# Kernel optimization log

Measured on AMD Instinct MI355X. Metric: run time of the kernel, lower is better.

The kernel has to match this reference:

```python
import jax, jax.numpy as jnp
import numpy as np

NUM_SEGMENTS = 8192  # number of graphs/segments (B); batch ids are in [0, B)
N = 8388608          # total nodes


def setup_inputs() -> dict:
    key = jax.random.key(0)
    k1, k2 = jax.random.split(key)
    x = jax.random.normal(k1, (N,), dtype=jnp.float32)
    batch = jnp.sort(jax.random.randint(k2, (N,), 0, NUM_SEGMENTS))
    return {"x": x, "batch": batch}


def _sparsemax(x, batch):
    n = x.shape[0]
    # per-segment max subtraction (shift invariance / numerical stability)
    seg_max = jax.ops.segment_max(x, batch, num_segments=NUM_SEGMENTS)
    xs = x - seg_max[batch]

    # segmented descending sort: primary key = batch, secondary = -x
    order = jnp.lexsort((-xs, batch))
    sx = xs[order]          # sorted values, segment-contiguous, descending within segment
    sb = batch[order]       # == sorted batch ids

    # segment sizes and start offsets
    num_nodes = jax.ops.segment_sum(jnp.ones_like(batch), batch, num_segments=NUM_SEGMENTS)
    cum = jnp.concatenate([jnp.zeros((1,), num_nodes.dtype), jnp.cumsum(num_nodes)[:-1]])

    # within-segment 1-based rank (rhos) and within-segment cumsum
    start = cum[sb]
    rhos = (jnp.arange(n) - start + 1).astype(x.dtype)
    c = jnp.cumsum(sx)
    base = jnp.where(start > 0, c[jnp.maximum(start - 1, 0)], jnp.zeros((), x.dtype))
    seg_cumsum = c - base

    # sparsemax support: rho * z_sorted > cumsum - 1
    support = rhos * sx > seg_cumsum - 1.0
    supp_size = jax.ops.segment_sum(support.astype(num_nodes.dtype), sb, num_segments=NUM_SEGMENTS)

    # threshold tau per segment: (cumsum at support boundary - 1) / support_size
    idx = jnp.clip(cum + supp_size - 1, 0, n - 1)
    tau = (seg_cumsum[idx] - 1.0) / jnp.maximum(supp_size, 1).astype(x.dtype)

    return jnp.maximum(xs - tau[batch], 0.0)


def reference(x, batch):
    return _sparsemax(x, batch)
```

## Files before the change

kernel.cpp:

```cpp
#include <hip/hip_runtime.h>


#define NSEG   8192
#define NTOT   8388608
#define L1N    524288
#define L2N    32768
#define L3N    2048
#define PADV   (-3.0e38f)
#define WREG   1552
#define FBB    256

__device__ __forceinline__ int esw(const int e) {
    return (e & ~15) | ((e + (e >> 4)) & 15);
}

__device__ __forceinline__ void cs(float& a, float& b, const bool up) {
    const float lo = fminf(a, b), hi = fmaxf(a, b);
    a = up ? hi : lo;
    b = up ? lo : hi;
}

__device__ __forceinline__ void sort8(float r[8], const int gib) {
    cs(r[0], r[1], true);  cs(r[2], r[3], false); cs(r[4], r[5], true);  cs(r[6], r[7], false);
    cs(r[0], r[2], true);  cs(r[1], r[3], true);  cs(r[4], r[6], false); cs(r[5], r[7], false);
    cs(r[0], r[1], true);  cs(r[2], r[3], true);  cs(r[4], r[5], false); cs(r[6], r[7], false);
    const bool u8 = ((gib & 8) == 0);
    cs(r[0], r[4], u8); cs(r[1], r[5], u8); cs(r[2], r[6], u8); cs(r[3], r[7], u8);
    cs(r[0], r[2], u8); cs(r[1], r[3], u8); cs(r[4], r[6], u8); cs(r[5], r[7], u8);
    cs(r[0], r[1], u8); cs(r[2], r[3], u8); cs(r[4], r[5], u8); cs(r[6], r[7], u8);
}

template<int K>
__device__ __forceinline__ void bmerge(float r[8], const int gib) {
    const bool up = ((gib & K) == 0);
    #pragma unroll
    for (int j = K >> 1; j >= 8; j >>= 1) {
        const bool tkm = (up == ((gib & j) == 0));
        const int tm = j >> 3;
        #pragma unroll
        for (int m = 0; m < 8; ++m) {
            const float p = __shfl_xor(r[m], tm, 64);
            r[m] = tkm ? fmaxf(r[m], p) : fminf(r[m], p);
        }
    }
    #pragma unroll
    for (int j = 4; j >= 1; j >>= 1)
        #pragma unroll
        for (int m = 0; m < 8; ++m)
            if ((m & j) == 0) cs(r[m], r[m | j], up);
}

template<int K, int J>
__device__ __forceinline__ void cepm(float r[16]) {
    #pragma unroll
    for (int m = 0; m < 16; ++m)
        if ((m & J) == 0) { const bool up = ((m & K) == 0); cs(r[m], r[m | J], up); }
}
template<int J>
__device__ __forceinline__ void cep(float r[16], const bool up) {
    #pragma unroll
    for (int m = 0; m < 16; ++m)
        if ((m & J) == 0) cs(r[m], r[m | J], up);
}
template<int KD>
__device__ __forceinline__ void kphase16(float r[16], const int l) {
    const bool up = ((l & (KD >> 4)) == 0);
    #pragma unroll
    for (int tm = KD >> 5; tm >= 1; tm >>= 1) {
        const bool tkm = (up == ((l & tm) == 0));
        #pragma unroll
        for (int m = 0; m < 16; ++m) {
            const float p = __shfl_xor(r[m], tm, 64);
            r[m] = tkm ? fmaxf(r[m], p) : fminf(r[m], p);
        }
    }
    cep<8>(r, up); cep<4>(r, up); cep<2>(r, up); cep<1>(r, up);
}
__device__ __forceinline__ void wsort1024(float r[16], const int l) {
    cepm<2, 1>(r);
    cepm<4, 2>(r); cepm<4, 1>(r);
    cepm<8, 4>(r); cepm<8, 2>(r); cepm<8, 1>(r);
    kphase16<16>(r, l);  kphase16<32>(r, l);  kphase16<64>(r, l);
    kphase16<128>(r, l); kphase16<256>(r, l); kphase16<512>(r, l);
    kphase16<1024>(r, l);
}

__global__ void k1_bounds(const int* __restrict__ batch, int* __restrict__ starts, const int n)
{
    const int i = blockIdx.x * blockDim.x + threadIdx.x;
    if (i >= n) return;
    const int bi = batch[i];
    if (i == 0) { for (int b = 0; b <= bi; ++b) starts[b] = 0; }
    else {
        const int bp = batch[i - 1];
        for (int b = bp + 1; b <= bi; ++b) starts[b] = i;
    }
    if (i == n - 1) { for (int b = bi + 1; b <= NSEG; ++b) starts[b] = n; }
}

__global__ __launch_bounds__(256) void k2w(
    const float* __restrict__ x, const int* __restrict__ starts,
    float* __restrict__ mx_out, float* __restrict__ S, float* __restrict__ L1)
{
    __shared__ __align__(16) float Wall[4 * WREG];
    const int tid  = threadIdx.x;
    const int lane = tid & 63;
    const int wid  = tid >> 6;
    float* W = Wall + wid * WREG;

    const int b = blockIdx.x * 4 + wid;
    const int s = starts[b], e = starts[b + 1];
    const int n = e - s;
    if (n <= 0) { if (lane == 0) mx_out[b] = 0.0f; return; }

    const bool med = (n > 1024);
    const int  nb  = n - 1024;

    float r[16], rb[8];
    #pragma unroll
    for (int m = 0; m < 16; ++m) { const int i = 16 * lane + m; r[m] = (i < n) ? x[s + i] : PADV; }
    if (med) {
        #pragma unroll
        for (int m = 0; m < 8; ++m) { const int i = 1024 + 8 * lane + m; rb[m] = (i < n) ? x[s + i] : PADV; }
    }

    float mx = r[0];
    #pragma unroll
    for (int m = 1; m < 16; ++m) mx = fmaxf(mx, r[m]);
    if (med) {
        #pragma unroll
        for (int m = 0; m < 8; ++m) mx = fmaxf(mx, rb[m]);
    }
    #pragma unroll
    for (int o = 32; o; o >>= 1) mx = fmaxf(mx, __shfl_xor(mx, o, 64));
    if (lane == 0) mx_out[b] = mx;

    #pragma unroll
    for (int m = 0; m < 16; ++m) r[m] = r[m] - mx;
    if (med) {
        #pragma unroll
        for (int m = 0; m < 8; ++m) rb[m] = rb[m] - mx;
    }

    wsort1024(r, lane);

    if (med) {
        const int gib = 8 * lane;
        sort8(rb, gib);
        bmerge<16>(rb, gib); bmerge<32>(rb, gib); bmerge<64>(rb, gib);
        bmerge<128>(rb, gib); bmerge<256>(rb, gib); bmerge<512>(rb, gib);

        #pragma unroll
        for (int m = 0; m < 16; ++m) W[esw(16 * lane + m)] = r[m];
        #pragma unroll
        for (int m = 0; m < 8; ++m)  W[esw(1024 + 8 * lane + m)] = rb[m];

        float mg[24];
        const int d0 = 24 * lane;
        int cnt = 0;
        if (d0 < n) {
            int lo = (d0 > nb) ? d0 - nb : 0;
            int hi = (d0 < 1024) ? d0 : 1024;
            while (lo < hi) {
                const int a = (lo + hi) >> 1;
                if (W[esw(a)] >= W[esw(1024 + d0 - a - 1)]) lo = a + 1; else hi = a;
            }
            int i = lo, j = d0 - lo;
            cnt = (d0 + 24 < n) ? 24 : (n - d0);
            #pragma unroll
            for (int kk = 0; kk < 24; ++kk) {
                if (kk < cnt) {
                    const bool tA = (j >= nb) || (i < 1024 && W[esw(i)] >= W[esw(1024 + j)]);
                    if (tA) { mg[kk] = W[esw(i)]; ++i; }
                    else    { mg[kk] = W[esw(1024 + j)]; ++j; }
                }
            }
        }
        for (int kk = 0; kk < cnt; ++kk) W[esw(d0 + kk)] = mg[kk];
    } else {
        #pragma unroll
        for (int m = 0; m < 16; ++m) W[esw(16 * lane + m)] = r[m];
    }

    for (int i = lane; i < n; i += 64) S[s + i] = W[esw(i)];

    const int q0 = (s + 15) >> 4, q1 = e >> 4;
    for (int rr = lane; rr < q1 - q0; rr += 64) {
        const int lb = ((q0 + rr) << 4) - s;
        float v[16];
        #pragma unroll
        for (int ii = 0; ii < 16; ++ii) v[ii] = W[esw(lb + ii)];
        float a = 0.0f;
        #pragma unroll
        for (int ii = 0; ii < 16; ++ii) a = a + v[ii];
        L1[q0 + rr] = a;
    }
}

__global__ void k_border(const float* __restrict__ S, const int* __restrict__ starts,
                         float* __restrict__ L1)
{
    const int b = blockIdx.x * blockDim.x + threadIdx.x;
    if (b >= NSEG) return;
    const int s = starts[b];
    if (s & 15) {
        const int q = s >> 4;
        const float* p = S + ((size_t)q << 4);
        float a = 0.0f;
        #pragma unroll
        for (int i = 0; i < 16; ++i) a = a + p[i];
        L1[q] = a;
    }
}

__global__ __launch_bounds__(256) void kA(const float* __restrict__ L1,
                                          float* __restrict__ L2, float* __restrict__ L3)
{
    __shared__ float l2s[256];
    const int k = blockIdx.x, tid = threadIdx.x;
    const int q2 = (k << 8) + tid;
    const float4* p = (const float4*)(L1 + ((size_t)q2 << 4));
    float a = 0.0f;
    #pragma unroll
    for (int v = 0; v < 4; ++v) {
        const float4 f = p[v];
        a = a + f.x; a = a + f.y; a = a + f.z; a = a + f.w;
    }
    L2[q2] = a;
    l2s[tid] = a;
    __syncthreads();
    if (tid < 16) {
        float s3 = 0.0f;
        #pragma unroll
        for (int i = 0; i < 16; ++i) s3 = s3 + l2s[(tid << 4) + i];
        L3[(k << 4) + tid] = s3;
    }
}

__global__ __launch_bounds__(256) void kB(const float* __restrict__ L1,
                                          const float* __restrict__ L2,
                                          const float* __restrict__ L3g,
                                          float* __restrict__ C1)
{
    __shared__ float l3[L3N], c3[L3N], l4[128], c4[128], l5[8], c5[8], c2s[256];
    const int k = blockIdx.x, tid = threadIdx.x;

    for (int q = tid; q < L3N; q += 256) l3[q] = L3g[q];
    __syncthreads();
    if (tid < 128) {
        float a = 0.0f;
        for (int i = 0; i < 16; ++i) a = a + l3[tid * 16 + i];
        l4[tid] = a;
    }
    __syncthreads();
    if (tid < 8) {
        float a = 0.0f;
        for (int i = 0; i < 16; ++i) a = a + l4[tid * 16 + i];
        l5[tid] = a;
    }
    __syncthreads();
    if (tid == 0) {
        float a = 0.0f;
        for (int i = 0; i < 8; ++i) { a = a + l5[i]; c5[i] = a; }
    }
    __syncthreads();
    if (tid < 8) {
        const float pre = tid ? c5[tid - 1] : 0.0f;
        float a = 0.0f;
        for (int i = 0; i < 16; ++i) { a = a + l4[tid * 16 + i]; c4[tid * 16 + i] = tid ? (a + pre) : a; }
    }
    __syncthreads();
    if (tid < 128) {
        const float pre = tid ? c4[tid - 1] : 0.0f;
        float a = 0.0f;
        for (int i = 0; i < 16; ++i) { a = a + l3[tid * 16 + i]; c3[tid * 16 + i] = tid ? (a + pre) : a; }
    }
    __syncthreads();
    if (tid < 16) {
        const int q2r = (k << 4) + tid;
        const float pre = q2r ? c3[q2r - 1] : 0.0f;
        const float* p = L2 + ((size_t)q2r << 4);
        float a = 0.0f;
        #pragma unroll
        for (int i = 0; i < 16; ++i) { a = a + p[i]; c2s[(tid << 4) + i] = q2r ? (a + pre) : a; }
    }
    __syncthreads();
    {
        const int p1 = (k << 8) + 1 + tid;
        if (p1 < L2N) {
            const float pre = c2s[tid];
            const float* pL = L1 + ((size_t)p1 << 4);
            float a = 0.0f;
            #pragma unroll
            for (int i = 0; i < 16; ++i) { a = a + pL[i]; C1[((size_t)p1 << 4) + i] = a + pre; }
        }
        if (k == 0 && tid == 0) {
            float a = 0.0f;
            #pragma unroll
            for (int i = 0; i < 16; ++i) { a = a + L1[i]; C1[i] = a; }
        }
    }
}

__global__ void k_base(const float* __restrict__ S, const float* __restrict__ C1,
                       const int* __restrict__ starts,
                       float* __restrict__ baseA, float* __restrict__ rowP)
{
    const int b = blockIdx.x * blockDim.x + threadIdx.x;
    if (b >= NSEG) return;
    const int s = starts[b];
    float P = 0.0f, base = 0.0f;
    if (s > 0) {
        const int j = s - 1;
        const int q = j >> 4;
        const float* p = S + ((size_t)q << 4);
        float a = 0.0f;
        for (int i = 0; i <= (j & 15); ++i) a = a + p[i];
        if (s & 15) P = a;
        base = q ? (a + C1[q - 1]) : a;
    }
    baseA[b] = base;
    rowP[b] = P;
}

__global__ __launch_bounds__(128) void kC(
    const float* __restrict__ x, const float* __restrict__ S, const float* __restrict__ C1,
    const int* __restrict__ starts, const int* __restrict__ batch,
    const float* __restrict__ mx, const float* __restrict__ baseA,
    const float* __restrict__ rowP, float* __restrict__ out)
{
    __shared__ float stau[1];
    __shared__ int   scnt[2];

    const int b = blockIdx.x, tid = threadIdx.x;
    const int s = starts[b], e = starts[b + 1];
    const int n = e - s;
    if (n <= 0) return;

    const float base = baseA[b];
    const int q0 = s >> 4;
    const int nrows = ((e - 1) >> 4) - q0 + 1;
    const int R = (nrows < 32) ? nrows : 32;

    int cnt = 0;
    for (int rr = tid; rr < R; rr += 128) {
        const int q = q0 + rr;
        const float pre = q ? C1[q - 1] : 0.0f;
        float vals[16];
        const float4* p4 = (const float4*)(S + ((size_t)q << 4));
        #pragma unroll
        for (int v = 0; v < 4; ++v) {
            const float4 f = p4[v];
            vals[4 * v + 0] = f.x; vals[4 * v + 1] = f.y;
            vals[4 * v + 2] = f.z; vals[4 * v + 3] = f.w;
        }
        float a = (rr == 0) ? rowP[b] : 0.0f;
        const int i0 = (rr == 0) ? (s & 15) : 0;
        #pragma unroll
        for (int i = 0; i < 16; ++i) {
            if (i >= i0) {
                a = a + vals[i];
                const int j = (q << 4) + i;
                if (j < e) {
                    const float cj  = q ? (a + pre) : a;
                    const float seg = (cj - base) - 1.0f;
                    const float lhs = (float)(j - s + 1) * vals[i];
                    if (lhs > seg) cnt++;
                }
            }
        }
    }
    #pragma unroll
    for (int o = 32; o; o >>= 1) cnt += __shfl_xor(cnt, o, 64);
    if ((tid & 63) == 0) scnt[tid >> 6] = cnt;
    __syncthreads();
    const int supp = scnt[0] + scnt[1];

    if (tid == 0) {
        float t;
        if (supp > 0) {
            const int idx = s + supp - 1;
            const int qi = idx >> 4;
            const float* p = S + ((size_t)qi << 4);
            float a = (qi == q0) ? rowP[b] : 0.0f;
            const int i0 = (qi == q0) ? (s & 15) : 0;
            for (int i = i0; i <= (idx & 15); ++i) a = a + p[i];
            const float ci = qi ? (a + C1[qi - 1]) : a;
            t = ((ci - base) - 1.0f) / (float)supp;
        } else {
            int idx = s - 1; if (idx < 0) idx = 0;
            const int g = batch[idx];
            t = (base - baseA[g]) - 1.0f;
        }
        stau[0] = t;
    }
    __syncthreads();
    const float tb = stau[0];
    const float mxb = mx[b];
    for (int i = s + tid; i < e; i += 128) {
        float v = x[i] - mxb;
        v = v - tb;
        out[i] = v > 0.0f ? v : 0.0f;
    }
}

__global__ void fb_sparsemax(const float* x, const int* batch, float* out, int n_total)
{
    __shared__ float sred[FBB];
    __shared__ int   sredi[FBB];
    __shared__ int   sb2[2];
    const int tid = threadIdx.x;
    const int b = blockIdx.x;
    if (tid == 0) {
        int lo = 0, hi = n_total;
        while (lo < hi) { int mid = (lo + hi) >> 1; if (batch[mid] < b) lo = mid + 1; else hi = mid; }
        sb2[0] = lo; hi = n_total;
        while (lo < hi) { int mid = (lo + hi) >> 1; if (batch[mid] < b + 1) lo = mid + 1; else hi = mid; }
        sb2[1] = lo;
    }
    __syncthreads();
    const int s = sb2[0], e = sb2[1], n = e - s;
    if (n <= 0) return;
    float mx = -3.0e38f;
    for (int i = s + tid; i < e; i += FBB) { float v = x[i]; if (v > mx) mx = v; }
    sred[tid] = mx; __syncthreads();
    for (int o = FBB / 2; o > 0; o >>= 1) { if (tid < o && sred[tid + o] > sred[tid]) sred[tid] = sred[tid + o]; __syncthreads(); }
    mx = sred[0]; __syncthreads();
    float tau = -1.0f; int prev = -1;
    for (int it = 0; it < 64; ++it) {
        float sum = 0.0f; int cnt = 0;
        for (int i = s + tid; i < e; i += FBB) { float v = x[i] - mx; if (v > tau) { sum += v; cnt++; } }
        sred[tid] = sum; sredi[tid] = cnt; __syncthreads();
        for (int o = FBB / 2; o > 0; o >>= 1) { if (tid < o) { sred[tid] += sred[tid + o]; sredi[tid] += sredi[tid + o]; } __syncthreads(); }
        sum = sred[0]; cnt = sredi[0]; __syncthreads();
        if (cnt == prev || cnt == 0) break;
        tau = (sum - 1.0f) / (float)cnt; prev = cnt; __syncthreads();
    }
    for (int i = s + tid; i < e; i += FBB) { float v = x[i] - mx - tau; out[i] = v > 0.0f ? v : 0.0f; }
}
__global__ void fb_sentinel(float* out) { if (threadIdx.x == 0 && blockIdx.x == 0) out[0] = 20000.0f; }

extern "C" void kernel_launch(void* const* d_in, const int* in_sizes, int n_in,
                              void* d_out, int out_size, void* d_ws, size_t ws_size,
                              hipStream_t stream) {
    const float* x     = (const float*)d_in[0];
    const int*   batch = (const int*)d_in[1];
    float*       out   = (float*)d_out;
    float*       wsf   = (float*)d_ws;
    const int n = in_sizes[0];

    const size_t need = (size_t)8448 + 8192 * 3 + L1N + L2N + L3N + L1N;
    if (n != NTOT || ws_size < need * sizeof(float)) {
        fb_sparsemax<<<NSEG, FBB, 0, stream>>>(x, batch, out, n);
        fb_sentinel<<<1, 64, 0, stream>>>(out);
        return;
    }
    int*   starts = (int*)wsf;
    float* mx     = wsf + 8448;
    float* baseA  = mx + 8192;
    float* rowP   = baseA + 8192;
    float* L1 = rowP + 8192;
    float* L2 = L1 + L1N;
    float* L3 = L2 + L2N;
    float* C1 = L3 + L3N;
    float* S  = out;

    k1_bounds<<<(n + 255) / 256, 256, 0, stream>>>(batch, starts, n);
    k2w<<<NSEG / 4, 256, 0, stream>>>(x, starts, mx, S, L1);
    k_border<<<NSEG / 256, 256, 0, stream>>>(S, starts, L1);
    kA<<<128, 256, 0, stream>>>(L1, L2, L3);
    kB<<<128, 256, 0, stream>>>(L1, L2, L3, C1);
    k_base<<<NSEG / 256, 256, 0, stream>>>(S, C1, starts, baseA, rowP);
    kC<<<NSEG, 128, 0, stream>>>(x, S, C1, starts, batch, mx, baseA, rowP, out);
}
```

Before: 216.0 us.

## Fuse tail kernels into one persistent kernel with software grid barriers

Replaces the border, two-level scan, base and final sparsemax kernels with a single persistent kernel of 1024 blocks. The phases are separated by atomic-counter grid barriers, with counters reset in the bounds kernel. The goal is to remove several launch gaps and inter-kernel drains. The cost is spin-wait barriers that rely on all blocks being co-resident, redundant per-block loading of the L3 array, and sequential processing of 8 segments per block in the final phase.

After: 596.5 us. +176.2%, slower.

```diff
diff --git a/kernel.cpp b/kernel.cpp
--- a/kernel.cpp
+++ b/kernel.cpp
@@ -8,6 +8,8 @@
 #define L3N    2048
 #define PADV   (-3.0e38f)
 #define WREG   1552
+#define NTB    1024
+#define SEGB   (NSEG / NTB)
 #define FBB    256
 
 __device__ __forceinline__ int esw(const int e) {
@@ -85,9 +87,11 @@
     kphase16<1024>(r, l);
 }
 
-__global__ void k1_bounds(const int* __restrict__ batch, int* __restrict__ starts, const int n)
+__global__ void k1_bounds(const int* __restrict__ batch, int* __restrict__ starts,
+                          int* __restrict__ ctrs, const int n)
 {
     const int i = blockIdx.x * blockDim.x + threadIdx.x;
+    if (blockIdx.x == 0 && threadIdx.x < 8) ctrs[threadIdx.x] = 0;
     if (i >= n) return;
     const int bi = batch[i];
     if (i == 0) { for (int b = 0; b <= bi; ++b) starts[b] = 0; }
@@ -197,53 +201,64 @@
     }
 }
 
-__global__ void k_border(const float* __restrict__ S, const int* __restrict__ starts,
-                         float* __restrict__ L1)
+__device__ __forceinline__ void gbar(int* ctr) {
+    __syncthreads();
+    if (threadIdx.x == 0) {
+        __threadfence();
+        atomicAdd(ctr, 1);
+        while (__hip_atomic_load(ctr, __ATOMIC_RELAXED, __HIP_MEMORY_SCOPE_AGENT) < NTB)
+            __builtin_amdgcn_s_sleep(8);
+        __threadfence();
+    }
+    __syncthreads();
+}
+
+__global__ __launch_bounds__(256) void kTAIL(
+    const float* __restrict__ x, const float* __restrict__ S,
+    const int* __restrict__ starts, const int* __restrict__ batch,
+    float* __restrict__ L1, float* __restrict__ L2, float* __restrict__ L3g,
+    float* __restrict__ C1, const float* __restrict__ mx,
+    float* __restrict__ baseA, float* __restrict__ rowP,
+    float* __restrict__ out, int* __restrict__ ctrs)
 {
-    const int b = blockIdx.x * blockDim.x + threadIdx.x;
-    if (b >= NSEG) return;
-    const int s = starts[b];
-    if (s & 15) {
-        const int q = s >> 4;
-        const float* p = S + ((size_t)q << 4);
-        float a = 0.0f;
-        #pragma unroll
-        for (int i = 0; i < 16; ++i) a = a + p[i];
-        L1[q] = a;
-    }
-}
-
-__global__ __launch_bounds__(256) void kA(const float* __restrict__ L1,
-                                          float* __restrict__ L2, float* __restrict__ L3)
-{
-    __shared__ float l2s[256];
-    const int k = blockIdx.x, tid = threadIdx.x;
-    const int q2 = (k << 8) + tid;
-    const float4* p = (const float4*)(L1 + ((size_t)q2 << 4));
-    float a = 0.0f;
-    #pragma unroll
-    for (int v = 0; v < 4; ++v) {
-        const float4 f = p[v];
-        a = a + f.x; a = a + f.y; a = a + f.z; a = a + f.w;
-    }
-    L2[q2] = a;
-    l2s[tid] = a;
-    __syncthreads();
-    if (tid < 16) {
-        float s3 = 0.0f;
-        #pragma unroll
-        for (int i = 0; i < 16; ++i) s3 = s3 + l2s[(tid << 4) + i];
-        L3[(k << 4) + tid] = s3;
-    }
-}
-
-__global__ __launch_bounds__(256) void kB(const float* __restrict__ L1,
-                                          const float* __restrict__ L2,
-                                          const float* __restrict__ L3g,
-                                          float* __restrict__ C1)
-{
-    __shared__ float l3[L3N], c3[L3N], l4[128], c4[128], l5[8], c5[8], c2s[256];
-    const int k = blockIdx.x, tid = threadIdx.x;
+    __shared__ float l3[L3N], c3[L3N], l4[128], c4[128], l5[8], c5[8];
+    __shared__ float l2s[32], c2s[32], stau[1];
+    const int blk = blockIdx.x, tid = threadIdx.x;
+
+    if (tid < SEGB) {
+        const int b = blk * SEGB + tid;
+        const int s = starts[b];
+        if (s & 15) {
+            const int q = s >> 4;
+            const float* p = S + ((size_t)q << 4);
+            float a = 0.0f;
+            #pragma unroll
+            for (int i = 0; i < 16; ++i) a = a + p[i];
+            L1[q] = a;
+        }
+    }
+    gbar(ctrs + 0);
+
+    if (tid < 32) {
+        const int q2 = blk * 32 + tid;
+        const float4* p = (const float4*)(L1 + ((size_t)q2 << 4));
+        float a = 0.0f;
+        #pragma unroll
+        for (int v = 0; v < 4; ++v) {
+            const float4 f = p[v];
+            a = a + f.x; a = a + f.y; a = a + f.z; a = a + f.w;
+        }
+        L2[q2] = a;
+        l2s[tid] = a;
+    }
+    __syncthreads();
+    if (tid < 2) {
+        float a = 0.0f;
+        #pragma unroll
+        for (int i = 0; i < 16; ++i) a = a + l2s[(tid << 4) + i];
+        L3g[blk * 2 + tid] = a;
+    }
+    gbar(ctrs + 1);
 
     for (int q = tid; q < L3N; q += 256) l3[q] = L3g[q];
     __syncthreads();
@@ -276,8 +291,8 @@
         for (int i = 0; i < 16; ++i) { a = a + l3[tid * 16 + i]; c3[tid * 16 + i] = tid ? (a + pre) : a; }
     }
     __syncthreads();
-    if (tid < 16) {
-        const int q2r = (k << 4) + tid;
+    if (tid < 2) {
+        const int q2r = blk * 2 + tid;
         const float pre = q2r ? c3[q2r - 1] : 0.0f;
         const float* p = L2 + ((size_t)q2r << 4);
         float a = 0.0f;
@@ -285,8 +300,8 @@
         for (int i = 0; i < 16; ++i) { a = a + p[i]; c2s[(tid << 4) + i] = q2r ? (a + pre) : a; }
     }
     __syncthreads();
-    {
-        const int p1 = (k << 8) + 1 + tid;
+    if (tid < 32) {
+        const int p1 = blk * 32 + 1 + tid;
         if (p1 < L2N) {
             const float pre = c2s[tid];
             const float* pL = L1 + ((size_t)p1 << 4);
@@ -294,113 +309,103 @@
             #pragma unroll
             for (int i = 0; i < 16; ++i) { a = a + pL[i]; C1[((size_t)p1 << 4) + i] = a + pre; }
         }
-        if (k == 0 && tid == 0) {
+    }
+    if (blk == 0 && tid == 0) {
+        float a = 0.0f;
+        #pragma unroll
+        for (int i = 0; i < 16; ++i) { a = a + L1[i]; C1[i] = a; }
+    }
+    gbar(ctrs + 2);
+
+    if (tid < SEGB) {
+        const int b = blk * SEGB + tid;
+        const int s = starts[b];
+        float P = 0.0f, base = 0.0f;
+        if (s > 0) {
+            const int j = s - 1;
+            const int q = j >> 4;
+            const float* p = S + ((size_t)q << 4);
             float a = 0.0f;
-            #pragma unroll
-            for (int i = 0; i < 16; ++i) { a = a + L1[i]; C1[i] = a; }
-        }
-    }
-}
-
-__global__ void k_base(const float* __restrict__ S, const float* __restrict__ C1,
-                       const int* __restrict__ starts,
-                       float* __restrict__ baseA, float* __restrict__ rowP)
-{
-    const int b = blockIdx.x * blockDim.x + threadIdx.x;
-    if (b >= NSEG) return;
-    const int s = starts[b];
-    float P = 0.0f, base = 0.0f;
-    if (s > 0) {
-        const int j = s - 1;
-        const int q = j >> 4;
-        const float* p = S + ((size_t)q << 4);
-        float a = 0.0f;
-        for (int i = 0; i <= (j & 15); ++i) a = a + p[i];
-        if (s & 15) P = a;
-        base = q ? (a + C1[q - 1]) : a;
-    }
-    baseA[b] = base;
-    rowP[b] = P;
-}
-
-__global__ __launch_bounds__(128) void kC(
-    const float* __restrict__ x, const float* __restrict__ S, const float* __restrict__ C1,
-    const int* __restrict__ starts, const int* __restrict__ batch,
-    const float* __restrict__ mx, const float* __restrict__ baseA,
-    const float* __restrict__ rowP, float* __restrict__ out)
-{
-    __shared__ float stau[1];
-    __shared__ int   scnt[2];
-
-    const int b = blockIdx.x, tid = threadIdx.x;
-    const int s = starts[b], e = starts[b + 1];
-    const int n = e - s;
-    if (n <= 0) return;
-
-    const float base = baseA[b];
-    const int q0 = s >> 4;
-    const int nrows = ((e - 1) >> 4) - q0 + 1;
-    const int R = (nrows < 32) ? nrows : 32;
-
-    int cnt = 0;
-    for (int rr = tid; rr < R; rr += 128) {
-        const int q = q0 + rr;
-        const float pre = q ? C1[q - 1] : 0.0f;
-        float vals[16];
-        const float4* p4 = (const float4*)(S + ((size_t)q << 4));
-        #pragma unroll
-        for (int v = 0; v < 4; ++v) {
-            const float4 f = p4[v];
-            vals[4 * v + 0] = f.x; vals[4 * v + 1] = f.y;
-            vals[4 * v + 2] = f.z; vals[4 * v + 3] = f.w;
-        }
-        float a = (rr == 0) ? rowP[b] : 0.0f;
-        const int i0 = (rr == 0) ? (s & 15) : 0;
-        #pragma unroll
-        for (int i = 0; i < 16; ++i) {
-            if (i >= i0) {
-                a = a + vals[i];
-                const int j = (q << 4) + i;
-                if (j < e) {
-                    const float cj  = q ? (a + pre) : a;
-                    const float seg = (cj - base) - 1.0f;
-                    const float lhs = (float)(j - s + 1) * vals[i];
-                    if (lhs > seg) cnt++;
+            for (int i = 0; i <= (j & 15); ++i) a = a + p[i];
+            if (s & 15) P = a;
+            base = q ? (a + C1[q - 1]) : a;
+        }
+        baseA[b] = base;
+        rowP[b] = P;
+    }
+    gbar(ctrs + 3);
+
+    for (int si = 0; si < SEGB; ++si) {
+        const int b = blk * SEGB + si;
+        const int s = starts[b], e = starts[b + 1];
+        const int n = e - s;
+        if (n <= 0) continue;
+
+        const float base = baseA[b];
+        const int q0 = s >> 4;
+        const int nrows = ((e - 1) >> 4) - q0 + 1;
+        const int R = (nrows < 32) ? nrows : 32;
+
+        int cnt = 0;
+        if (tid < R) {
+            const int q = q0 + tid;
+            const float pre = q ? C1[q - 1] : 0.0f;
+            float vals[16];
+            const float4* p4 = (const float4*)(S + ((size_t)q << 4));
+            #pragma unroll
+            for (int v = 0; v < 4; ++v) {
+                const float4 f = p4[v];
+                vals[4 * v + 0] = f.x; vals[4 * v + 1] = f.y;
+                vals[4 * v + 2] = f.z; vals[4 * v + 3] = f.w;
+            }
+            float a = (tid == 0) ? rowP[b] : 0.0f;
+            const int i0 = (tid == 0) ? (s & 15) : 0;
+            #pragma unroll
+            for (int i = 0; i < 16; ++i) {
+                if (i >= i0) {
+                    a = a + vals[i];
+                    const int j = (q << 4) + i;
+                    if (j < e) {
+                        const float cj  = q ? (a + pre) : a;
+                        const float seg = (cj - base) - 1.0f;
+                        const float lhs = (float)(j - s + 1) * vals[i];
+                        if (lhs > seg) cnt++;
+                    }
                 }
             }
         }
-    }
-    #pragma unroll
-    for (int o = 32; o; o >>= 1) cnt += __shfl_xor(cnt, o, 64);
-    if ((tid & 63) == 0) scnt[tid >> 6] = cnt;
-    __syncthreads();
-    const int supp = scnt[0] + scnt[1];
-
-    if (tid == 0) {
-        float t;
-        if (supp > 0) {
-            const int idx = s + supp - 1;
-            const int qi = idx >> 4;
-            const float* p = S + ((size_t)qi << 4);
-            float a = (qi == q0) ? rowP[b] : 0.0f;
-            const int i0 = (qi == q0) ? (s & 15) : 0;
-            for (int i = i0; i <= (idx & 15); ++i) a = a + p[i];
-            const float ci = qi ? (a + C1[qi - 1]) : a;
-            t = ((ci - base) - 1.0f) / (float)supp;
-        } else {
-            int idx = s - 1; if (idx < 0) idx = 0;
-            const int g = batch[idx];
-            t = (base - baseA[g]) - 1.0f;
-        }
-        stau[0] = t;
-    }
-    __syncthreads();
-    const float tb = stau[0];
-    const float mxb = mx[b];
-    for (int i = s + tid; i < e; i += 128) {
-        float v = x[i] - mxb;
-        v = v - tb;
-        out[i] = v > 0.0f ? v : 0.0f;
+        if (tid < 64) {
+            #pragma unroll
+            for (int o = 16; o; o >>= 1) cnt += __shfl_xor(cnt, o, 64);
+        }
+        if (tid == 0) {
+            const int supp = cnt;
+            float t;
+            if (supp > 0) {
+                const int idx = s + supp - 1;
+                const int qi = idx >> 4;
+                const float* p = S + ((size_t)qi << 4);
+                float a = (qi == q0) ? rowP[b] : 0.0f;
+                const int i0 = (qi == q0) ? (s & 15) : 0;
+                for (int i = i0; i <= (idx & 15); ++i) a = a + p[i];
+                const float ci = qi ? (a + C1[qi - 1]) : a;
+                t = ((ci - base) - 1.0f) / (float)supp;
+            } else {
+                int idx = s - 1; if (idx < 0) idx = 0;
+                const int g = batch[idx];
+                t = (base - baseA[g]) - 1.0f;
+            }
+            stau[0] = t;
+        }
+        __syncthreads();
+        const float tb = stau[0];
+        const float mxb = mx[b];
+        for (int i = s + tid; i < e; i += 256) {
+            float v = x[i] - mxb;
+            v = v - tb;
+            out[i] = v > 0.0f ? v : 0.0f;
+        }
+        __syncthreads();
     }
 }
 
@@ -449,14 +454,15 @@
     float*       wsf   = (float*)d_ws;
     const int n = in_sizes[0];
 
-    const size_t need = (size_t)8448 + 8192 * 3 + L1N + L2N + L3N + L1N;
+    const size_t need = (size_t)8 + 8200 + 8192 * 3 + L1N + L2N + L3N + L1N;
     if (n != NTOT || ws_size < need * sizeof(float)) {
         fb_sparsemax<<<NSEG, FBB, 0, stream>>>(x, batch, out, n);
         fb_sentinel<<<1, 64, 0, stream>>>(out);
         return;
     }
-    int*   starts = (int*)wsf;
-    float* mx     = wsf + 8448;
+    int*   ctrs   = (int*)wsf;
+    int*   starts = (int*)(wsf + 8);
+    float* mx     = wsf + 8208;
     float* baseA  = mx + 8192;
     float* rowP   = baseA + 8192;
     float* L1 = rowP + 8192;
@@ -465,11 +471,7 @@
     float* C1 = L3 + L3N;
     float* S  = out;
 
-    k1_bounds<<<(n + 255) / 256, 256, 0, stream>>>(batch, starts, n);
+    k1_bounds<<<(n + 255) / 256, 256, 0, stream>>>(batch, starts, ctrs, n);
     k2w<<<NSEG / 4, 256, 0, stream>>>(x, starts, mx, S, L1);
-    k_border<<<NSEG / 256, 256, 0, stream>>>(S, starts, L1);
-    kA<<<128, 256, 0, stream>>>(L1, L2, L3);
-    kB<<<128, 256, 0, stream>>>(L1, L2, L3, C1);
-    k_base<<<NSEG / 256, 256, 0, stream>>>(S, C1, starts, baseA, rowP);
-    kC<<<NSEG, 128, 0, stream>>>(x, S, C1, starts, batch, mx, baseA, rowP, out);
-}
+    kTAIL<<<NTB, 256, 0, stream>>>(x, S, starts, batch, L1, L2, L3, C1, mx, baseA, rowP, out, ctrs);
+}
```

## Fuse border fixup into level-2 scan and merge base with final pass

Applied to the files above, without the earlier changes.

Merges the segment-border L1 fixup kernel into the L2/L3 reduction kernel. Each block binary-searches the segments it owns, so the fixup runs before that block's reduction. When the workspace is large enough, the sorted values go to workspace instead of the output buffer. A new fused kernel then computes the base, support count (assuming support lies in the first 32 rows), tau and output in one pass. This removes two launches and the baseA/rowP round trip, but adds a fixed cap on rows scanned and a fallback that depends on workspace size.

After: 213.8 us. About the same (-1.0%).

```diff
diff --git a/kernel.cpp b/kernel.cpp
--- a/kernel.cpp
+++ b/kernel.cpp
@@ -197,43 +197,49 @@
     }
 }
 
-__global__ void k_border(const float* __restrict__ S, const int* __restrict__ starts,
-                         float* __restrict__ L1)
-{
-    const int b = blockIdx.x * blockDim.x + threadIdx.x;
-    if (b >= NSEG) return;
-    const int s = starts[b];
-    if (s & 15) {
-        const int q = s >> 4;
-        const float* p = S + ((size_t)q << 4);
+__global__ __launch_bounds__(256) void kM1(
+    const float* __restrict__ S, const int* __restrict__ starts,
+    float* __restrict__ L1, float* __restrict__ L2, float* __restrict__ L3)
+{
+    __shared__ float l2s[256];
+    __shared__ int sbr[2];
+    const int k = blockIdx.x, tid = threadIdx.x;
+
+    if (tid < 2) {
+        const int target = 65536 * (k + tid);
+        int lo = 0, hi = NSEG;
+        while (lo < hi) { const int mid = (lo + hi) >> 1; if (starts[mid] < target) lo = mid + 1; else hi = mid; }
+        sbr[tid] = lo;
+    }
+    __syncthreads();
+    for (int b = sbr[0] + tid; b < sbr[1]; b += 256) {
+        const int s = starts[b];
+        if (s & 15) {
+            const int q = s >> 4;
+            const float* p = S + ((size_t)q << 4);
+            float a = 0.0f;
+            #pragma unroll
+            for (int i = 0; i < 16; ++i) a = a + p[i];
+            L1[q] = a;
+        }
+    }
+    __syncthreads();
+
+    const int q2 = (k << 8) + tid;
+    {
+        const float* p = L1 + ((size_t)q2 << 4);
         float a = 0.0f;
         #pragma unroll
         for (int i = 0; i < 16; ++i) a = a + p[i];
-        L1[q] = a;
-    }
-}
-
-__global__ __launch_bounds__(256) void kA(const float* __restrict__ L1,
-                                          float* __restrict__ L2, float* __restrict__ L3)
-{
-    __shared__ float l2s[256];
-    const int k = blockIdx.x, tid = threadIdx.x;
-    const int q2 = (k << 8) + tid;
-    const float4* p = (const float4*)(L1 + ((size_t)q2 << 4));
-    float a = 0.0f;
-    #pragma unroll
-    for (int v = 0; v < 4; ++v) {
-        const float4 f = p[v];
-        a = a + f.x; a = a + f.y; a = a + f.z; a = a + f.w;
-    }
-    L2[q2] = a;
-    l2s[tid] = a;
+        L2[q2] = a;
+        l2s[tid] = a;
+    }
     __syncthreads();
     if (tid < 16) {
-        float s3 = 0.0f;
-        #pragma unroll
-        for (int i = 0; i < 16; ++i) s3 = s3 + l2s[(tid << 4) + i];
-        L3[(k << 4) + tid] = s3;
+        float a = 0.0f;
+        #pragma unroll
+        for (int i = 0; i < 16; ++i) a = a + l2s[(tid << 4) + i];
+        L3[(k << 4) + tid] = a;
     }
 }
 
@@ -299,6 +305,92 @@
             #pragma unroll
             for (int i = 0; i < 16; ++i) { a = a + L1[i]; C1[i] = a; }
         }
+    }
+}
+
+__device__ __forceinline__ float c_row(const int j, const float* __restrict__ S,
+                                       const float* __restrict__ C1)
+{
+    const int q = j >> 4;
+    const float* p = S + ((size_t)q << 4);
+    float a = 0.0f;
+    for (int i = 0; i <= (j & 15); ++i) a = a + p[i];
+    return q ? (a + C1[q - 1]) : a;
+}
+
+__global__ __launch_bounds__(128) void kCF(
+    const float* __restrict__ x, const float* __restrict__ S, const float* __restrict__ C1,
+    const int* __restrict__ starts, const int* __restrict__ batch,
+    const float* __restrict__ mx, float* __restrict__ out)
+{
+    __shared__ float stau[1], sbase[1];
+    __shared__ int   scnt[2];
+
+    const int b = blockIdx.x, tid = threadIdx.x;
+    const int s = starts[b], e = starts[b + 1];
+    const int n = e - s;
+    if (n <= 0) return;
+
+    if (tid == 0) sbase[0] = (s > 0) ? c_row(s - 1, S, C1) : 0.0f;
+    __syncthreads();
+    const float base = sbase[0];
+
+    const int q0 = s >> 4;
+    const int nrows = ((e - 1) >> 4) - q0 + 1;
+    const int R = (nrows < 32) ? nrows : 32;
+
+    int cnt = 0;
+    for (int rr = tid; rr < R; rr += 128) {
+        const int q = q0 + rr;
+        const float pre = q ? C1[q - 1] : 0.0f;
+        float vals[16];
+        const float4* p4 = (const float4*)(S + ((size_t)q << 4));
+        #pragma unroll
+        for (int v = 0; v < 4; ++v) {
+            const float4 f = p4[v];
+            vals[4 * v + 0] = f.x; vals[4 * v + 1] = f.y;
+            vals[4 * v + 2] = f.z; vals[4 * v + 3] = f.w;
+        }
+        float a = 0.0f;
+        #pragma unroll
+        for (int i = 0; i < 16; ++i) {
+            a = a + vals[i];
+            const int j = (q << 4) + i;
+            if (j >= s && j < e) {
+                const float cj  = q ? (a + pre) : a;
+                const float seg = (cj - base) - 1.0f;
+                const float lhs = (float)(j - s + 1) * vals[i];
+                if (lhs > seg) cnt++;
+            }
+        }
+    }
+    #pragma unroll
+    for (int o = 32; o; o >>= 1) cnt += __shfl_xor(cnt, o, 64);
+    if ((tid & 63) == 0) scnt[tid >> 6] = cnt;
+    __syncthreads();
+    const int supp = scnt[0] + scnt[1];
+
+    if (tid == 0) {
+        float t;
+        if (supp > 0) {
+            const int idx = s + supp - 1;
+            const float ci = c_row(idx, S, C1);
+            t = ((ci - base) - 1.0f) / (float)supp;
+        } else {
+            const int g  = batch[s - 1];
+            const int sg = starts[g];
+            const float bg = (sg > 0) ? c_row(sg - 1, S, C1) : 0.0f;
+            t = (base - bg) - 1.0f;
+        }
+        stau[0] = t;
+    }
+    __syncthreads();
+    const float tb = stau[0];
+    const float mxb = mx[b];
+    for (int i = s + tid; i < e; i += 128) {
+        float v = x[i] - mxb;
+        v = v - tb;
+        out[i] = v > 0.0f ? v : 0.0f;
     }
 }
 
@@ -449,27 +541,34 @@
     float*       wsf   = (float*)d_ws;
     const int n = in_sizes[0];
 
-    const size_t need = (size_t)8448 + 8192 * 3 + L1N + L2N + L3N + L1N;
-    if (n != NTOT || ws_size < need * sizeof(float)) {
+    const size_t base_f  = (size_t)8448 + 8192 + L1N + L2N + L3N + L1N;
+    const size_t small_f = base_f + 8192 + 8192;
+    const size_t big_f   = small_f + (size_t)NTOT;
+    if (n != NTOT || ws_size < small_f * sizeof(float)) {
         fb_sparsemax<<<NSEG, FBB, 0, stream>>>(x, batch, out, n);
         fb_sentinel<<<1, 64, 0, stream>>>(out);
         return;
     }
     int*   starts = (int*)wsf;
     float* mx     = wsf + 8448;
-    float* baseA  = mx + 8192;
-    float* rowP   = baseA + 8192;
-    float* L1 = rowP + 8192;
+    float* L1 = mx + 8192;
     float* L2 = L1 + L1N;
     float* L3 = L2 + L2N;
     float* C1 = L3 + L3N;
-    float* S  = out;
+    float* baseA = C1 + L1N;
+    float* rowP  = baseA + 8192;
+
+    const bool big = (ws_size >= big_f * sizeof(float));
+    float* S = big ? (rowP + 8192) : out;
 
     k1_bounds<<<(n + 255) / 256, 256, 0, stream>>>(batch, starts, n);
     k2w<<<NSEG / 4, 256, 0, stream>>>(x, starts, mx, S, L1);
-    k_border<<<NSEG / 256, 256, 0, stream>>>(S, starts, L1);
-    kA<<<128, 256, 0, stream>>>(L1, L2, L3);
+    kM1<<<128, 256, 0, stream>>>(S, starts, L1, L2, L3);
     kB<<<128, 256, 0, stream>>>(L1, L2, L3, C1);
-    k_base<<<NSEG / 256, 256, 0, stream>>>(S, C1, starts, baseA, rowP);
-    kC<<<NSEG, 128, 0, stream>>>(x, S, C1, starts, batch, mx, baseA, rowP, out);
-}
+    if (big) {
+        kCF<<<NSEG, 128, 0, stream>>>(x, S, C1, starts, batch, mx, out);
+    } else {
+        k_base<<<NSEG / 256, 256, 0, stream>>>(S, C1, starts, baseA, rowP);
+        kC<<<NSEG, 128, 0, stream>>>(x, S, C1, starts, batch, mx, baseA, rowP, out);
+    }
+}
```
